# Performance work log

Hardware: AMD Instinct MI355X
Metric: run time of the kernel (lower is better)

Reference implementation:

```python
import jax, jax.numpy as jnp
import numpy as np

IN_FEATURES = 4096
OUT_FEATURES = 4096
CODESZ = 8
CODEBOOK_SIZE = 256


def fwht(x):
    """Normalized fast Walsh-Hadamard transform over the last dim (power of 2).
    Equivalent to x @ (H / sqrt(n)); H symmetric so this serves both
    matmul_hadUt and matmul_hadU in the power-of-2 case (had=None, K=1)."""
    orig_shape = x.shape
    n = orig_shape[-1]
    x = x.reshape(-1, n)
    h = 2
    while h <= n:
        x = x.reshape(-1, n // h, 2, h // 2)
        a, b = x[..., 0, :], x[..., 1, :]
        x = jnp.stack([a + b, a - b], axis=-2)
        h *= 2
    x = x.reshape(orig_shape)
    return x * (1.0 / np.sqrt(n)).astype(np.float32)


def setup_inputs() -> dict:
    key = jax.random.key(0)
    k1, k2, k3, k4, k5, k6 = jax.random.split(key, 6)
    x = jax.random.normal(k1, (4, 2048, IN_FEATURES), dtype=jnp.float32)
    Qidxs = jax.random.randint(k2, (OUT_FEATURES, IN_FEATURES // CODESZ), 0, CODEBOOK_SIZE, dtype=jnp.int32)
    grid = jax.random.normal(k3, (CODEBOOK_SIZE, CODESZ), dtype=jnp.float32)
    SU = jax.random.uniform(k4, (IN_FEATURES,), dtype=jnp.float32)
    SV = jax.random.uniform(k5, (OUT_FEATURES,), dtype=jnp.float32)
    bias = jax.random.normal(k6, (OUT_FEATURES,), dtype=jnp.float32)
    return {"x": x, "Qidxs": Qidxs, "grid": grid, "SU": SU, "SV": SV, "bias": bias}


def reference(x, Qidxs, grid, SU, SV, bias):
    lead = x.shape[:-1]
    h = x.reshape(-1, IN_FEATURES)            # [T, in]
    h = h * SU                                 # scale by SU
    h = fwht(h)                                # matmul_hadUt (input rotation)
    # codebook dequant: gather code vectors and form W_hat [out, in]
    W_hat = grid[Qidxs].reshape(OUT_FEATURES, IN_FEATURES)
    y = h @ W_hat.T                            # [T, out]
    y = fwht(y)[:, :OUT_FEATURES]              # matmul_hadU (output rotation)
    y = y * SV
    y = y.reshape(*lead, OUT_FEATURES) + bias
    return y
```

## Files before the change

### kernel.cpp

```cpp
#include <hip/hip_runtime.h>

#define IN_F 4096
#define OUT_F 4096
#define NROWS 8192
#define BK 32
#define NT (IN_F / BK)

typedef __attribute__((ext_vector_type(4))) float f32x4;
typedef __attribute__((ext_vector_type(8))) short bf16x8;
typedef __attribute__((ext_vector_type(8))) unsigned short u16x8;

__device__ __forceinline__ unsigned short f2bf(float f) {
  union { float f; unsigned u; } x; x.f = f;
  unsigned r = x.u + 0x7FFFu + ((x.u >> 16) & 1u);
  return (unsigned short)(r >> 16);
}

__device__ __forceinline__ void gload_lds16(const unsigned short* g, unsigned short* l) {
  __builtin_amdgcn_global_load_lds((__attribute__((address_space(1))) void*)g,
                                   (__attribute__((address_space(3))) void*)l,
                                   16, 0, 0);
}

__device__ __forceinline__ void bfly16(float v[16]) {
#pragma unroll
  for (int s = 1; s < 16; s <<= 1) {
#pragma unroll
    for (int i = 0; i < 16; ++i) {
      if (!(i & s)) { float a = v[i], b = v[i + s]; v[i] = a + b; v[i + s] = a - b; }
    }
  }
}

__global__ __launch_bounds__(256) void dequant_kernel(const int* __restrict__ Q,
                                                      const float* __restrict__ grid,
                                                      unsigned short* __restrict__ Wb) {
  int g = blockIdx.x * 256 + threadIdx.x;
  int idx = Q[g];
  const f32x4* gp = (const f32x4*)(grid + idx * 8);
  f32x4 v0 = gp[0], v1 = gp[1];
  u16x8 o;
  o[0] = f2bf(v0[0]); o[1] = f2bf(v0[1]); o[2] = f2bf(v0[2]); o[3] = f2bf(v0[3]);
  o[4] = f2bf(v1[0]); o[5] = f2bf(v1[1]); o[6] = f2bf(v1[2]); o[7] = f2bf(v1[3]);
  *(u16x8*)(Wb + (size_t)g * 8) = o;
}

__global__ __launch_bounds__(256) void fwht1_kernel(const float* __restrict__ x,
                                                    const float* __restrict__ SU,
                                                    unsigned short* __restrict__ Hb) {
  __shared__ float buf[4096];
  int tid = threadIdx.x;
  size_t rbase = (size_t)blockIdx.x * IN_F;
  const f32x4* x4 = (const f32x4*)(x + rbase);
  const f32x4* su4 = (const f32x4*)SU;
  f32x4* b4 = (f32x4*)buf;
#pragma unroll
  for (int s = 0; s < 4; ++s) {
    int c = tid + 256 * s;
    f32x4 v = x4[c];
    f32x4 u = su4[c];
    v.x *= u.x; v.y *= u.y; v.z *= u.z; v.w *= u.w;
    b4[c] = v;
  }
  __syncthreads();
  float v[16];
  {
#pragma unroll
    for (int j = 0; j < 4; ++j) {
      f32x4 t4 = b4[tid * 4 + j];
      v[j*4+0] = t4.x; v[j*4+1] = t4.y; v[j*4+2] = t4.z; v[j*4+3] = t4.w;
    }
    bfly16(v);
#pragma unroll
    for (int j = 0; j < 4; ++j) {
      f32x4 t4; t4.x = v[j*4+0]; t4.y = v[j*4+1]; t4.z = v[j*4+2]; t4.w = v[j*4+3];
      b4[tid * 4 + j] = t4;
    }
  }
  __syncthreads();
  {
    int lo = tid & 15, hi = tid >> 4;
    int base = lo + (hi << 8);
#pragma unroll
    for (int j = 0; j < 16; ++j) v[j] = buf[base + (j << 4)];
    bfly16(v);
#pragma unroll
    for (int j = 0; j < 16; ++j) buf[base + (j << 4)] = v[j];
  }
  __syncthreads();
  {
#pragma unroll
    for (int j = 0; j < 16; ++j) v[j] = buf[tid + (j << 8)];
    bfly16(v);
#pragma unroll
    for (int j = 0; j < 16; ++j)
      Hb[rbase + tid + (j << 8)] = f2bf(v[j] * 0.015625f);
  }
}

#define MM(i, A, B) acc[i] = __builtin_amdgcn_mfma_f32_16x16x32_bf16(A, B, acc[i], 0, 0, 0)

__global__ __launch_bounds__(512) void gemm256_kernel(const unsigned short* __restrict__ Hb,
                                                      const unsigned short* __restrict__ Wb,
                                                      float* __restrict__ Y) {
  __shared__ unsigned short lds[4][2][256 * BK];
  const int tid = threadIdx.x;
  const int lane = tid & 63;
  const int wid = tid >> 6;
  const int wr = wid >> 2;
  const int wc = wid & 3;
  const int lrow = lane & 15;
  const int kgrp = lane >> 4;

  const int bid = blockIdx.x;
  const int swz = (bid & 7) * 64 + (bid >> 3);
  const int brow = (swz >> 4) << 8;
  const int bcol = (swz & 15) << 8;

  const unsigned short* Ab = Hb + (size_t)brow * IN_F;
  const unsigned short* Bb = Wb + (size_t)bcol * IN_F;

  const int r0 = tid >> 2;
  const int sc = ((tid & 3) ^ ((r0 >> 1) & 3)) << 3;
  const unsigned short* Ag0 = Ab + (size_t)r0 * IN_F + sc;
  const unsigned short* Ag1 = Ab + (size_t)(r0 + 128) * IN_F + sc;
  const unsigned short* Bg0 = Bb + (size_t)r0 * IN_F + sc;
  const unsigned short* Bg1 = Bb + (size_t)(r0 + 128) * IN_F + sc;

#define STAGE_A(t, s) { gload_lds16(Ag0 + (t) * BK, &lds[s][0][tid * 8]); \
                        gload_lds16(Ag1 + (t) * BK, &lds[s][0][(tid + 512) * 8]); }
#define STAGE_B(t, s) { gload_lds16(Bg0 + (t) * BK, &lds[s][1][tid * 8]); \
                        gload_lds16(Bg1 + (t) * BK, &lds[s][1][(tid + 512) * 8]); }

  auto fragLd = [&](const unsigned short* base, int R) -> bf16x8 {
    return *(const bf16x8*)(base + R * BK + ((kgrp ^ ((R >> 1) & 3)) << 3));
  };

  const int ar = wr * 128 + lrow;
  const int br = wc * 64 + lrow;

  f32x4 acc[32] = {};
  bf16x8 a0, a1, a2, a3, b0, b1, b2, b3;

  STAGE_A(0, 0); STAGE_B(0, 0);
  STAGE_A(1, 1); STAGE_B(1, 1);
  STAGE_A(2, 2); STAGE_B(2, 2);
  asm volatile("s_waitcnt vmcnt(8)" ::: "memory");
  __builtin_amdgcn_s_barrier();

  for (int t = 0; t < NT; ++t) {
    const int s = t & 3;
    const unsigned short* As = &lds[s][0][0];
    const unsigned short* Bs = &lds[s][1][0];

    a0 = fragLd(As, ar +  0); a1 = fragLd(As, ar + 16);
    a2 = fragLd(As, ar + 32); a3 = fragLd(As, ar + 48);
    b0 = fragLd(Bs, br +  0); b1 = fragLd(Bs, br + 16);
    b2 = fragLd(Bs, br + 32); b3 = fragLd(Bs, br + 48);
    if (t + 3 < NT) STAGE_A(t + 3, (t + 3) & 3);
    __builtin_amdgcn_s_barrier();
    asm volatile("s_waitcnt lgkmcnt(0)" ::: "memory");
    __builtin_amdgcn_sched_barrier(0);
    __builtin_amdgcn_s_setprio(1);
    MM( 0, a0, b0); MM( 1, a0, b1); MM( 2, a0, b2); MM( 3, a0, b3);
    MM( 4, a1, b0); MM( 5, a1, b1); MM( 6, a1, b2); MM( 7, a1, b3);
    MM( 8, a2, b0); MM( 9, a2, b1); MM(10, a2, b2); MM(11, a2, b3);
    MM(12, a3, b0); MM(13, a3, b1); MM(14, a3, b2); MM(15, a3, b3);
    __builtin_amdgcn_s_setprio(0);
    __builtin_amdgcn_s_barrier();

    a0 = fragLd(As, ar +  64); a1 = fragLd(As, ar +  80);
    a2 = fragLd(As, ar +  96); a3 = fragLd(As, ar + 112);
    if (t + 3 < NT) STAGE_B(t + 3, (t + 3) & 3);
    __builtin_amdgcn_s_barrier();
    asm volatile("s_waitcnt lgkmcnt(0)" ::: "memory");
    __builtin_amdgcn_sched_barrier(0);
    __builtin_amdgcn_s_setprio(1);
    MM(16, a0, b0); MM(17, a0, b1); MM(18, a0, b2); MM(19, a0, b3);
    MM(20, a1, b0); MM(21, a1, b1); MM(22, a1, b2); MM(23, a1, b3);
    MM(24, a2, b0); MM(25, a2, b1); MM(26, a2, b2); MM(27, a2, b3);
    MM(28, a3, b0); MM(29, a3, b1); MM(30, a3, b2); MM(31, a3, b3);
    __builtin_amdgcn_s_setprio(0);
    if (t <= NT - 4)      { asm volatile("s_waitcnt vmcnt(8)" ::: "memory"); }
    else if (t == NT - 3) { asm volatile("s_waitcnt vmcnt(4)" ::: "memory"); }
    else if (t == NT - 2) { asm volatile("s_waitcnt vmcnt(0)" ::: "memory"); }
    __builtin_amdgcn_s_barrier();
  }

#pragma unroll
  for (int mf = 0; mf < 8; ++mf) {
    int grow = brow + wr * 128 + mf * 16 + kgrp * 4;
    float* yp = Y + (size_t)grow * OUT_F + bcol + wc * 64 + lrow;
#pragma unroll
    for (int r = 0; r < 4; ++r)
#pragma unroll
      for (int n = 0; n < 4; ++n)
        yp[(size_t)r * OUT_F + n * 16] = acc[mf * 4 + n][r];
  }
#undef STAGE_A
#undef STAGE_B
}

__global__ __launch_bounds__(256) void fwht2_kernel(float* __restrict__ Y,
                                                    const float* __restrict__ SV,
                                                    const float* __restrict__ bias) {
  __shared__ float buf[4096];
  int tid = threadIdx.x;
  size_t rbase = (size_t)blockIdx.x * OUT_F;
  f32x4* y4 = (f32x4*)(Y + rbase);
  f32x4* b4 = (f32x4*)buf;
#pragma unroll
  for (int s = 0; s < 4; ++s) {
    int c = tid + 256 * s;
    b4[c] = y4[c];
  }
  __syncthreads();
  float v[16];
  {
#pragma unroll
    for (int j = 0; j < 4; ++j) {
      f32x4 t4 = b4[tid * 4 + j];
      v[j*4+0] = t4.x; v[j*4+1] = t4.y; v[j*4+2] = t4.z; v[j*4+3] = t4.w;
    }
    bfly16(v);
#pragma unroll
    for (int j = 0; j < 4; ++j) {
      f32x4 t4; t4.x = v[j*4+0]; t4.y = v[j*4+1]; t4.z = v[j*4+2]; t4.w = v[j*4+3];
      b4[tid * 4 + j] = t4;
    }
  }
  __syncthreads();
  {
    int lo = tid & 15, hi = tid >> 4;
    int base = lo + (hi << 8);
#pragma unroll
    for (int j = 0; j < 16; ++j) v[j] = buf[base + (j << 4)];
    bfly16(v);
#pragma unroll
    for (int j = 0; j < 16; ++j) buf[base + (j << 4)] = v[j];
  }
  __syncthreads();
  {
#pragma unroll
    for (int j = 0; j < 16; ++j) v[j] = buf[tid + (j << 8)];
    bfly16(v);
#pragma unroll
    for (int j = 0; j < 16; ++j) {
      int col = tid + (j << 8);
      Y[rbase + col] = v[j] * 0.015625f * SV[col] + bias[col];
    }
  }
}

extern "C" void kernel_launch(void* const* d_in, const int* in_sizes, int n_in,
                              void* d_out, int out_size, void* d_ws, size_t ws_size,
                              hipStream_t stream) {
  const float* x     = (const float*)d_in[0];
  const int*   Qidxs = (const int*)d_in[1];
  const float* grid  = (const float*)d_in[2];
  const float* SU    = (const float*)d_in[3];
  const float* SV    = (const float*)d_in[4];
  const float* bias  = (const float*)d_in[5];
  float* out = (float*)d_out;

  unsigned short* Wb = (unsigned short*)d_ws;
  unsigned short* Hb = Wb + (size_t)OUT_F * IN_F;

  hipLaunchKernelGGL(dequant_kernel, dim3((OUT_F * (IN_F / 8)) / 256), dim3(256), 0, stream,
                     Qidxs, grid, Wb);
  hipLaunchKernelGGL(fwht1_kernel, dim3(NROWS), dim3(256), 0, stream, x, SU, Hb);
  hipLaunchKernelGGL(gemm256_kernel, dim3((NROWS / 256) * (OUT_F / 256)), dim3(512), 0, stream,
                     Hb, Wb, out);
  hipLaunchKernelGGL(fwht2_kernel, dim3(NROWS), dim3(256), 0, stream, out, SV, bias);
}
```

Baseline: 343.8 us.

## Use a 3-stage LDS ring with prefetch distance 2 and one barrier per K-step

```diff
diff --git a/kernel.cpp b/kernel.cpp
--- a/kernel.cpp
+++ b/kernel.cpp
@@ -98,12 +98,10 @@
   }
 }
 
-#define MM(i, A, B) acc[i] = __builtin_amdgcn_mfma_f32_16x16x32_bf16(A, B, acc[i], 0, 0, 0)
-
 __global__ __launch_bounds__(512) void gemm256_kernel(const unsigned short* __restrict__ Hb,
                                                       const unsigned short* __restrict__ Wb,
                                                       float* __restrict__ Y) {
-  __shared__ unsigned short lds[4][2][256 * BK];
+  __shared__ unsigned short lds[3][2][256 * BK];
   const int tid = threadIdx.x;
   const int lane = tid & 63;
   const int wid = tid >> 6;
@@ -117,20 +115,19 @@
   const int brow = (swz >> 4) << 8;
   const int bcol = (swz & 15) << 8;
 
-  const unsigned short* Ab = Hb + (size_t)brow * IN_F;
-  const unsigned short* Bb = Wb + (size_t)bcol * IN_F;
-
   const int r0 = tid >> 2;
   const int sc = ((tid & 3) ^ ((r0 >> 1) & 3)) << 3;
-  const unsigned short* Ag0 = Ab + (size_t)r0 * IN_F + sc;
-  const unsigned short* Ag1 = Ab + (size_t)(r0 + 128) * IN_F + sc;
-  const unsigned short* Bg0 = Bb + (size_t)r0 * IN_F + sc;
-  const unsigned short* Bg1 = Bb + (size_t)(r0 + 128) * IN_F + sc;
-
-#define STAGE_A(t, s) { gload_lds16(Ag0 + (t) * BK, &lds[s][0][tid * 8]); \
-                        gload_lds16(Ag1 + (t) * BK, &lds[s][0][(tid + 512) * 8]); }
-#define STAGE_B(t, s) { gload_lds16(Bg0 + (t) * BK, &lds[s][1][tid * 8]); \
-                        gload_lds16(Bg1 + (t) * BK, &lds[s][1][(tid + 512) * 8]); }
+  const unsigned short* AgR0 = Hb + (size_t)(brow + r0) * IN_F + sc;
+  const unsigned short* AgR1 = Hb + (size_t)(brow + r0 + 128) * IN_F + sc;
+  const unsigned short* BgR0 = Wb + (size_t)(bcol + r0) * IN_F + sc;
+  const unsigned short* BgR1 = Wb + (size_t)(bcol + r0 + 128) * IN_F + sc;
+
+#define STAGE_A(t) { \
+  gload_lds16(AgR0 + (t) * BK, &lds[(t) % 3][0][tid * 8]); \
+  gload_lds16(AgR1 + (t) * BK, &lds[(t) % 3][0][(tid + 512) * 8]); }
+#define STAGE_B(t) { \
+  gload_lds16(BgR0 + (t) * BK, &lds[(t) % 3][1][tid * 8]); \
+  gload_lds16(BgR1 + (t) * BK, &lds[(t) % 3][1][(tid + 512) * 8]); }
 
   auto fragLd = [&](const unsigned short* base, int R) -> bf16x8 {
     return *(const bf16x8*)(base + R * BK + ((kgrp ^ ((R >> 1) & 3)) << 3));
@@ -139,66 +136,73 @@
   const int ar = wr * 128 + lrow;
   const int br = wc * 64 + lrow;
 
+#define MM(i, A, B) acc[i] = __builtin_amdgcn_mfma_f32_16x16x32_bf16(A, B, acc[i], 0, 0, 0)
+#define BURST1 { \
+  asm volatile("s_waitcnt lgkmcnt(0)" ::: "memory"); \
+  __builtin_amdgcn_sched_barrier(0); \
+  __builtin_amdgcn_s_setprio(1); \
+  MM( 0, a0, b0); MM( 1, a0, b1); MM( 2, a0, b2); MM( 3, a0, b3); \
+  MM( 4, a1, b0); MM( 5, a1, b1); MM( 6, a1, b2); MM( 7, a1, b3); \
+  MM( 8, a2, b0); MM( 9, a2, b1); MM(10, a2, b2); MM(11, a2, b3); \
+  MM(12, a3, b0); MM(13, a3, b1); MM(14, a3, b2); MM(15, a3, b3); \
+  __builtin_amdgcn_s_setprio(0); }
+#define BURST2 { \
+  asm volatile("s_waitcnt lgkmcnt(0)" ::: "memory"); \
+  __builtin_amdgcn_sched_barrier(0); \
+  __builtin_amdgcn_s_setprio(1); \
+  MM(16, a0, b0); MM(17, a0, b1); MM(18, a0, b2); MM(19, a0, b3); \
+  MM(20, a1, b0); MM(21, a1, b1); MM(22, a1, b2); MM(23, a1, b3); \
+  MM(24, a2, b0); MM(25, a2, b1); MM(26, a2, b2); MM(27, a2, b3); \
+  MM(28, a3, b0); MM(29, a3, b1); MM(30, a3, b2); MM(31, a3, b3); \
+  __builtin_amdgcn_s_setprio(0); }
+
   f32x4 acc[32] = {};
   bf16x8 a0, a1, a2, a3, b0, b1, b2, b3;
 
-  STAGE_A(0, 0); STAGE_B(0, 0);
-  STAGE_A(1, 1); STAGE_B(1, 1);
-  STAGE_A(2, 2); STAGE_B(2, 2);
-  asm volatile("s_waitcnt vmcnt(8)" ::: "memory");
+  STAGE_A(0); STAGE_B(0);
+  STAGE_A(1); STAGE_B(1);
+  asm volatile("s_waitcnt vmcnt(4)" ::: "memory");
   __builtin_amdgcn_s_barrier();
 
   for (int t = 0; t < NT; ++t) {
-    const int s = t & 3;
+    const int s = t % 3;
     const unsigned short* As = &lds[s][0][0];
     const unsigned short* Bs = &lds[s][1][0];
+    const bool pf = (t + 2 < NT);
 
     a0 = fragLd(As, ar +  0); a1 = fragLd(As, ar + 16);
     a2 = fragLd(As, ar + 32); a3 = fragLd(As, ar + 48);
     b0 = fragLd(Bs, br +  0); b1 = fragLd(Bs, br + 16);
     b2 = fragLd(Bs, br + 32); b3 = fragLd(Bs, br + 48);
-    if (t + 3 < NT) STAGE_A(t + 3, (t + 3) & 3);
-    __builtin_amdgcn_s_barrier();
-    asm volatile("s_waitcnt lgkmcnt(0)" ::: "memory");
-    __builtin_amdgcn_sched_barrier(0);
-    __builtin_amdgcn_s_setprio(1);
-    MM( 0, a0, b0); MM( 1, a0, b1); MM( 2, a0, b2); MM( 3, a0, b3);
-    MM( 4, a1, b0); MM( 5, a1, b1); MM( 6, a1, b2); MM( 7, a1, b3);
-    MM( 8, a2, b0); MM( 9, a2, b1); MM(10, a2, b2); MM(11, a2, b3);
-    MM(12, a3, b0); MM(13, a3, b1); MM(14, a3, b2); MM(15, a3, b3);
-    __builtin_amdgcn_s_setprio(0);
-    __builtin_amdgcn_s_barrier();
+    if (pf) STAGE_A(t + 2);
+    BURST1;
 
     a0 = fragLd(As, ar +  64); a1 = fragLd(As, ar +  80);
     a2 = fragLd(As, ar +  96); a3 = fragLd(As, ar + 112);
-    if (t + 3 < NT) STAGE_B(t + 3, (t + 3) & 3);
-    __builtin_amdgcn_s_barrier();
-    asm volatile("s_waitcnt lgkmcnt(0)" ::: "memory");
-    __builtin_amdgcn_sched_barrier(0);
-    __builtin_amdgcn_s_setprio(1);
-    MM(16, a0, b0); MM(17, a0, b1); MM(18, a0, b2); MM(19, a0, b3);
-    MM(20, a1, b0); MM(21, a1, b1); MM(22, a1, b2); MM(23, a1, b3);
-    MM(24, a2, b0); MM(25, a2, b1); MM(26, a2, b2); MM(27, a2, b3);
-    MM(28, a3, b0); MM(29, a3, b1); MM(30, a3, b2); MM(31, a3, b3);
-    __builtin_amdgcn_s_setprio(0);
-    if (t <= NT - 4)      { asm volatile("s_waitcnt vmcnt(8)" ::: "memory"); }
-    else if (t == NT - 3) { asm volatile("s_waitcnt vmcnt(4)" ::: "memory"); }
+    if (pf) STAGE_B(t + 2);
+    BURST2;
+
+    if (t < NT - 2)       { asm volatile("s_waitcnt vmcnt(4)" ::: "memory"); }
     else if (t == NT - 2) { asm volatile("s_waitcnt vmcnt(0)" ::: "memory"); }
-    __builtin_amdgcn_s_barrier();
+    if (t < NT - 1) __builtin_amdgcn_s_barrier();
   }
 
 #pragma unroll
   for (int mf = 0; mf < 8; ++mf) {
     int grow = brow + wr * 128 + mf * 16 + kgrp * 4;
     float* yp = Y + (size_t)grow * OUT_F + bcol + wc * 64 + lrow;
+    int ai = (mf >> 2) * 16 + (mf & 3) * 4;
 #pragma unroll
     for (int r = 0; r < 4; ++r)
 #pragma unroll
-      for (int n = 0; n < 4; ++n)
-        yp[(size_t)r * OUT_F + n * 16] = acc[mf * 4 + n][r];
+      for (int nf = 0; nf < 4; ++nf)
+        yp[(size_t)r * OUT_F + nf * 16] = acc[ai + nf][r];
   }
 #undef STAGE_A
 #undef STAGE_B
+#undef MM
+#undef BURST1
+#undef BURST2
 }
 
 __global__ __launch_bounds__(256) void fwht2_kernel(float* __restrict__ Y,
```

Result: faster. 328.0 us (-4.6%).
